# Optimization experiments

Hardware: AMD Instinct MI355X
Metric: run time of the kernel (lower is better)

Reference implementation:

```python
import jax, jax.numpy as jnp
import numpy as np

WAY, SHOT, P, FDIM, HDIM, NHEADS = 5, 5, 10, 640, 512, 8
H = W = 14
NUM_SPT = WAY * SHOT
EPS_BN = 1e-5
EPS_LN = 1e-5


def _l2norm(x, axis=-1):
    n = jnp.linalg.norm(x, axis=axis, keepdims=True)
    return x / jnp.maximum(n, 1e-12)


def _cbr(x, Wc, bc, g, beta):
    # 1x1 conv + BatchNorm(train stats) + ReLU. x: [N,C,H,W], Wc: [O,C]
    y = jnp.einsum('nchw,oc->nohw', x, Wc) + bc[None, :, None, None]
    mu = y.mean((0, 2, 3))
    var = y.var((0, 2, 3))
    y = (y - mu[None, :, None, None]) / jnp.sqrt(var[None, :, None, None] + EPS_BN)
    y = y * g[None, :, None, None] + beta[None, :, None, None]
    return jax.nn.relu(y)


def _mha(x, Wq, bq, Wk, bk, Wv, bv, Wa, ba, ln_g, ln_b):
    B, S, D = x.shape
    dk = D // NHEADS
    def proj(Wt, bt):
        return (x @ Wt.T + bt).reshape(B, S, NHEADS, dk).transpose(0, 2, 1, 3)
    q, k, v = proj(Wq, bq), proj(Wk, bk), proj(Wv, bv)
    scores = jnp.einsum('bhqd,bhkd->bhqk', q, k) / jnp.sqrt(jnp.asarray(dk, x.dtype))
    att = jax.nn.softmax(scores, axis=-1)
    ctx = jnp.einsum('bhqk,bhkd->bhqd', att, v).transpose(0, 2, 1, 3).reshape(B, S, D)
    out = ctx @ Wa.T + ba + x  # residual
    mu = out.mean(-1, keepdims=True)
    var = out.var(-1, keepdims=True)
    return ((out - mu) / jnp.sqrt(var + EPS_LN)) * ln_g + ln_b


def setup_inputs() -> dict:
    k = jax.random.key(0)
    ks = jax.random.split(k, 16)
    s = 0.02
    return {
        'key':   jax.random.normal(ks[0], (NUM_SPT + 75, FDIM, H, W), jnp.float32),
        'query': jax.random.normal(ks[1], (75, FDIM, H, W), jnp.float32),
        'Wc':  jax.random.normal(ks[2], (HDIM, FDIM), jnp.float32) * s,
        'bc':  jnp.zeros((HDIM,), jnp.float32),
        'g1':  jnp.ones((HDIM,), jnp.float32),
        'b1':  jnp.zeros((HDIM,), jnp.float32),
        'Wq':  jax.random.normal(ks[3], (HDIM, HDIM), jnp.float32) * s,
        'bq':  jnp.zeros((HDIM,), jnp.float32),
        'Wk':  jax.random.normal(ks[4], (HDIM, HDIM), jnp.float32) * s,
        'bk':  jnp.zeros((HDIM,), jnp.float32),
        'Wv':  jax.random.normal(ks[5], (HDIM, HDIM), jnp.float32) * s,
        'bv':  jnp.zeros((HDIM,), jnp.float32),
        'Wa':  jax.random.normal(ks[6], (HDIM, HDIM), jnp.float32) * s,
        'ba':  jnp.zeros((HDIM,), jnp.float32),
        'ln_g': jnp.ones((HDIM,), jnp.float32),
        'ln_b': jnp.zeros((HDIM,), jnp.float32),
        'Wm':  jax.random.normal(ks[7], (P, HDIM), jnp.float32) * s,
        'Wo':  jax.random.normal(ks[8], (FDIM, HDIM), jnp.float32) * s,
        'bo':  jnp.zeros((FDIM,), jnp.float32),
        'g2':  jnp.ones((FDIM,), jnp.float32),
        'b2':  jnp.zeros((FDIM,), jnp.float32),
    }


def reference(key, query, Wc, bc, g1, b1, Wq, bq, Wk, bk, Wv, bv, Wa, ba, ln_g, ln_b, Wm, Wo, bo, g2, b2):
    # proto_concept: conv1x1 + BN + ReLU
    key_ = _cbr(key, Wc, bc, g1, b1)                 # [B, HDIM, H, W]
    B, D, h, w = key_.shape
    feats = key_.transpose(0, 2, 3, 1).reshape(B, h * w, D)
    support = feats[:NUM_SPT].reshape(SHOT, WAY, h * w, D).mean(0)   # [WAY, hw, D]
    qf = feats[NUM_SPT:]                                             # [NQ, hw, D]
    nq = B - NUM_SPT

    support = _mha(support, Wq, bq, Wk, bk, Wv, bv, Wa, ba, ln_g, ln_b)
    qf = _mha(qf, Wq, bq, Wk, bk, Wv, bv, Wa, ba, ln_g, ln_b)

    # prototype formation: softmax over all support positions (dim 0)
    mw = (support @ Wm.T).reshape(-1, P, 1)          # [WAY*hw, P, 1]
    mw = jax.nn.softmax(mw, axis=0)
    sflat = support.reshape(-1, D)                   # [WAY*hw, D]
    protos = (mw * sflat[:, None, :]).sum(0)         # [P, D]

    # ---- query_loss (training branch) ----
    protos_n = _l2norm(protos)                       # [P, D]

    # diversity loss (faithful to original incl. triu over (P, D) dims)
    diff2 = (protos_n[None, :, :] - protos_n[:, None, :]) ** 2   # [P, P, D]
    dis = 1.0 - diff2[None]                                      # [1, P, P, D]
    dis = dis * (dis > 0).astype(dis.dtype)
    tri = jnp.triu(jnp.ones((P, D), dis.dtype), k=1)
    dis = dis * tri
    dis_loss = (dis.sum(1).sum(1) * 2.0 / (P * (P - 1))).mean()

    cst_loss = ((protos_n[1:] - protos_n[:-1]) ** 2).sum(-1).mean()

    # dual-softmax scoring (protos shared across batch)
    score = jnp.einsum('bnd,md->bnm', qf, protos_n)  # [NQ, hw, P]
    sp = jax.nn.softmax(score, axis=-1)
    new_q = _l2norm(jnp.einsum('bnm,md->bnd', sp, protos_n))

    idx = jnp.argmax(score, axis=-1)                 # top-1 proto per position
    pos = protos_n[idx]                              # [NQ, hw, D]
    fea_loss = jnp.mean((qf - pos) ** 2)

    uq = new_q.transpose(0, 2, 1).reshape(nq, D, h, w)
    updated = _cbr(uq, Wo, bo, g2, b2) + query       # [NQ, FDIM, H, W]
    return (updated, fea_loss, cst_loss, dis_loss)
```

## Files before the change

kernel.cpp:

```cpp
#include <hip/hip_runtime.h>
#include <math.h>

#define WAYS 5
#define SHOTS 5
#define PP 10
#define FDIMC 640
#define HD 512
#define SEQ 196
#define NB 100
#define NQB 75
#define NMHA 80
#define M1 (NB*SEQ)
#define MMHA (NMHA*SEQ)
#define MQ (NQB*SEQ)
#define NBLK_ROWK (MQ/4)
#define OUT_UPD (NQB*FDIMC*SEQ)

#define OFF_CS1S 0
#define OFF_CS1Q 512
#define OFF_CS2S 1024
#define OFF_CS2Q 1664
#define ZERO_FLOATS 2306
#define OFF_ST1SC 2308
#define OFF_ST1SH 2820
#define OFF_ST2SC 3332
#define OFF_ST2SH 3972
#define OFF_M    4612
#define OFF_PN   14412

#define RB 20480
#define RC (RB + 15439360)
#define RD (RC + 8028160)
#define RE (RD + 8028160)
#define RF (RE + 8028160)
#define RG (RF + 4014080)
#define RH (RG + 4014080)
#define OFF_XOUT (RB + 10000000)
#define OFF_FEAP (RF + 3763200)
#define OFF_WSM  RG
#define OFF_PPART (RG + 16384)

typedef __bf16 bf16x8 __attribute__((ext_vector_type(8)));
typedef float f32x4 __attribute__((ext_vector_type(4)));

__device__ __forceinline__ ushort f2bf(float f) {
  unsigned u = __float_as_uint(f);
  return (ushort)((u + 0x7fffu + ((u >> 16) & 1u)) >> 16);
}
__device__ __forceinline__ float bf2f(ushort u) {
  return __uint_as_float(((unsigned)u) << 16);
}

__device__ __forceinline__ f32x4 mfma16(bf16x8 a, bf16x8 b, f32x4 c) {
  return __builtin_amdgcn_mfma_f32_16x16x32_bf16(a, b, c, 0, 0, 0);
}

__device__ __forceinline__ float waveSum(float v) {
#pragma unroll
  for (int o = 32; o; o >>= 1) v += __shfl_xor(v, o, 64);
  return v;
}


__global__ __launch_bounds__(256) void key_transpose(const float* __restrict__ key,
                                                     ushort* __restrict__ keyT) {
  __shared__ float T[32][33];
  const int n = blockIdx.z, c0 = blockIdx.y*32, s0 = blockIdx.x*32;
  const int tj = threadIdx.x & 31, ti = threadIdx.x >> 5;
#pragma unroll
  for (int it = 0; it < 4; ++it) {
    const int cl = it*8 + ti;
    const int s = s0 + tj;
    T[cl][tj] = (s < SEQ) ? key[((size_t)n*FDIMC + c0 + cl)*SEQ + s] : 0.f;
  }
  __syncthreads();
#pragma unroll
  for (int it = 0; it < 4; ++it) {
    const int sl = it*8 + ti;
    const int s = s0 + sl;
    if (s < SEQ) keyT[((size_t)(n*SEQ + s))*FDIMC + c0 + tj] = f2bf(T[tj][sl]);
  }
}

__global__ void wconvert(const float* __restrict__ Wc, const float* __restrict__ Wq,
                         const float* __restrict__ Wk, const float* __restrict__ Wv,
                         const float* __restrict__ Wa, const float* __restrict__ Wo,
                         ushort* __restrict__ wh) {
  const int i = blockIdx.x*256 + threadIdx.x;
  float v;
  if (i < 327680) v = Wc[i];
  else if (i < 589824) v = Wq[i - 327680];
  else if (i < 851968) v = Wk[i - 589824];
  else if (i < 1114112) v = Wv[i - 851968];
  else if (i < 1376256) v = Wa[i - 1114112];
  else v = Wo[i - 1376256];
  wh[i] = f2bf(v);
}

template<int OM, int CS>
__global__ __launch_bounds__(256) void gemm_bf(const ushort* __restrict__ A,
    const ushort* __restrict__ W, const float* __restrict__ bias,
    float* __restrict__ Cf, ushort* __restrict__ Ch, int M, int N, int K,
    float* __restrict__ gsum, float* __restrict__ gsq) {
  __shared__ ushort As[128*32];
  __shared__ ushort Bs[128*32];
  __shared__ float csum[128], csq[128];
  const int tid = threadIdx.x;
  const int m0 = blockIdx.y*128, n0 = blockIdx.x*128;
  const int w = tid >> 6, lane = tid & 63;
  const int wr = w >> 1, wc = w & 1;
  const int g = lane >> 4, c = lane & 15;

  const int ch0 = tid, ch1 = 256 + tid;
  const int ar0 = ch0 >> 2, ar1 = ch1 >> 2;
  const int ak0 = (ch0 & 3) * 8, ak1 = (ch1 & 3) * 8;
  int gr0 = m0 + ar0; if (gr0 > M-1) gr0 = M-1;
  int gr1 = m0 + ar1; if (gr1 > M-1) gr1 = M-1;
  const ushort* Ap0 = A + (size_t)gr0*K + ak0;
  const ushort* Ap1 = A + (size_t)gr1*K + ak1;
  const ushort* Wp0 = W + (size_t)(n0 + ar0)*K + ak0;
  const ushort* Wp1 = W + (size_t)(n0 + ar1)*K + ak1;

  f32x4 acc[4][4];
#pragma unroll
  for (int i = 0; i < 4; ++i)
#pragma unroll
    for (int j = 0; j < 4; ++j) acc[i][j] = (f32x4)(0.0f);

  for (int k0 = 0; k0 < K; k0 += 32) {
    const uint4 a0 = *(const uint4*)(Ap0 + k0);
    const uint4 a1 = *(const uint4*)(Ap1 + k0);
    const uint4 b0 = *(const uint4*)(Wp0 + k0);
    const uint4 b1 = *(const uint4*)(Wp1 + k0);
    __syncthreads();
    *(uint4*)(&As[ch0*8]) = a0;
    *(uint4*)(&As[ch1*8]) = a1;
    *(uint4*)(&Bs[ch0*8]) = b0;
    *(uint4*)(&Bs[ch1*8]) = b1;
    __syncthreads();
    bf16x8 af[4], bfr[4];
#pragma unroll
    for (int mi = 0; mi < 4; ++mi)
      af[mi] = *(const bf16x8*)(&As[(wr*64 + mi*16 + c)*32 + g*8]);
#pragma unroll
    for (int ni = 0; ni < 4; ++ni)
      bfr[ni] = *(const bf16x8*)(&Bs[(wc*64 + ni*16 + c)*32 + g*8]);
#pragma unroll
    for (int mi = 0; mi < 4; ++mi)
#pragma unroll
      for (int ni = 0; ni < 4; ++ni)
        acc[mi][ni] = mfma16(af[mi], bfr[ni], acc[mi][ni]);
  }

  if (CS) {
    __syncthreads();
    if (tid < 128) { csum[tid] = 0.f; csq[tid] = 0.f; }
    __syncthreads();
  }

#pragma unroll
  for (int ni = 0; ni < 4; ++ni) {
    const int col = n0 + wc*64 + ni*16 + c;
    const float bb = bias[col];
    float ls = 0.f, lq = 0.f;
#pragma unroll
    for (int mi = 0; mi < 4; ++mi) {
#pragma unroll
      for (int q = 0; q < 4; ++q) {
        const int row = m0 + wr*64 + mi*16 + g*4 + q;
        if (row < M) {
          const float v = acc[mi][ni][q] + bb;
          if (OM == 0) Cf[(size_t)row*N + col] = v;
          else if (OM == 1) Ch[(size_t)row*N + col] = f2bf(v);
          else Ch[(size_t)row*N + col] = f2bf(v*0.125f);
          if (CS) { ls += v; lq += v*v; }
        }
      }
    }
    if (CS) {
      const int lcol = wc*64 + ni*16 + c;
      atomicAdd(&csum[lcol], ls);
      atomicAdd(&csq[lcol], lq);
    }
  }
  if (CS) {
    __syncthreads();
    if (tid < 128) {
      atomicAdd(&gsum[n0 + tid], csum[tid]);
      atomicAdd(&gsq[n0 + tid], csq[tid]);
    }
  }
}


__global__ void bn_finalize(const float* __restrict__ sums, const float* __restrict__ sumsq,
    const float* __restrict__ g, const float* __restrict__ b, int C, float invM,
    float* __restrict__ scale, float* __restrict__ shift) {
  const int c = blockIdx.x*256 + threadIdx.x;
  if (c >= C) return;
  const float mu = sums[c]*invM;
  const float var = sumsq[c]*invM - mu*mu;
  const float sc = rsqrtf(var + 1e-5f) * g[c];
  scale[c] = sc;
  shift[c] = b[c] - mu*sc;
}

__global__ __launch_bounds__(256) void bn1_apply(const ushort* __restrict__ y1,
    const float* __restrict__ scale, const float* __restrict__ shift,
    ushort* __restrict__ srawh, ushort* __restrict__ xbufh) {
  const int i8 = blockIdx.x*256 + threadIdx.x;
  if (i8 >= M1*HD/8) return;
  const int e = i8 << 3;
  const int col = e & (HD - 1);
  const uint4 raw = ((const uint4*)y1)[i8];
  unsigned rw[4] = {raw.x, raw.y, raw.z, raw.w};
  unsigned res[4];
#pragma unroll
  for (int j = 0; j < 4; ++j) {
    float v0 = bf2f((ushort)(rw[j] & 0xffffu));
    float v1 = bf2f((ushort)(rw[j] >> 16));
    v0 = fmaxf(fmaf(v0, scale[col + 2*j],     shift[col + 2*j]),     0.f);
    v1 = fmaxf(fmaf(v1, scale[col + 2*j + 1], shift[col + 2*j + 1]), 0.f);
    res[j] = (unsigned)f2bf(v0) | ((unsigned)f2bf(v1) << 16);
  }
  const uint4 o = make_uint4(res[0], res[1], res[2], res[3]);
  if (e < 25*SEQ*HD) ((uint4*)srawh)[i8] = o;
  else ((uint4*)xbufh)[i8 - (20*SEQ*HD/8)] = o;
}

__global__ void support_mean(const ushort* __restrict__ srawh, ushort* __restrict__ xbufh) {
  const int i8 = blockIdx.x*256 + threadIdx.x;
  if (i8 >= WAYS*SEQ*HD/8) return;
  const int e = i8 << 3;
  const int w = e / (SEQ*HD);
  const int rem = e - w*(SEQ*HD);
  float acc[8] = {};
#pragma unroll
  for (int s = 0; s < SHOTS; ++s) {
    const uint4 v = *(const uint4*)(srawh + (size_t)(s*WAYS + w)*(SEQ*HD) + rem);
    const unsigned rw[4] = {v.x, v.y, v.z, v.w};
#pragma unroll
    for (int j = 0; j < 4; ++j) {
      acc[2*j]   += bf2f((ushort)(rw[j] & 0xffffu));
      acc[2*j+1] += bf2f((ushort)(rw[j] >> 16));
    }
  }
  unsigned res[4];
#pragma unroll
  for (int j = 0; j < 4; ++j)
    res[j] = (unsigned)f2bf(acc[2*j]*0.2f) | ((unsigned)f2bf(acc[2*j+1]*0.2f) << 16);
  ((uint4*)xbufh)[i8] = make_uint4(res[0], res[1], res[2], res[3]);
}


__global__ __launch_bounds__(256) void attn_qk(const ushort* __restrict__ qb,
    const ushort* __restrict__ kb, ushort* __restrict__ P) {
  __shared__ ushort Ks[208*72];
  const int bh = blockIdx.x, b = bh >> 3, h = bh & 7;
  const int tid = threadIdx.x;
  for (int idx = tid; idx < 208*8; idx += 256) {
    const int row = idx >> 3, part = idx & 7;
    uint4 v = make_uint4(0u,0u,0u,0u);
    if (row < SEQ) v = *(const uint4*)(kb + ((size_t)(b*SEQ + row))*HD + h*64 + part*8);
    *(uint4*)(&Ks[row*72 + part*8]) = v;
  }
  __syncthreads();
  const int w = tid >> 6, lane = tid & 63, g = lane >> 4, c = lane & 15;
  for (int rt = w; rt < 13; rt += 4) {
    int qrow = b*SEQ + rt*16 + c; if (qrow > MMHA-1) qrow = MMHA-1;
    const bf16x8 aq0 = *(const bf16x8*)(qb + (size_t)qrow*HD + h*64 + g*8);
    const bf16x8 aq1 = *(const bf16x8*)(qb + (size_t)qrow*HD + h*64 + 32 + g*8);
    f32x4 acc[13];
#pragma unroll
    for (int ct = 0; ct < 13; ++ct) acc[ct] = (f32x4)(0.0f);
#pragma unroll
    for (int ct = 0; ct < 13; ++ct) {
      const bf16x8 b0 = *(const bf16x8*)(&Ks[(ct*16 + c)*72 + g*8]);
      const bf16x8 b1 = *(const bf16x8*)(&Ks[(ct*16 + c)*72 + 32 + g*8]);
      acc[ct] = mfma16(aq0, b0, acc[ct]);
      acc[ct] = mfma16(aq1, b1, acc[ct]);
    }
    if (c >= 4) acc[12] = (f32x4)(-1e30f);
    float mrow[4], Z[4];
#pragma unroll
    for (int q = 0; q < 4; ++q) {
      float mx = acc[0][q];
#pragma unroll
      for (int ct = 1; ct < 13; ++ct) mx = fmaxf(mx, acc[ct][q]);
      mrow[q] = mx;
    }
#pragma unroll
    for (int q = 0; q < 4; ++q) {
#pragma unroll
      for (int msk = 1; msk < 16; msk <<= 1)
        mrow[q] = fmaxf(mrow[q], __shfl_xor(mrow[q], msk, 64));
    }
#pragma unroll
    for (int q = 0; q < 4; ++q) Z[q] = 0.f;
#pragma unroll
    for (int ct = 0; ct < 13; ++ct)
#pragma unroll
      for (int q = 0; q < 4; ++q) {
        const float e = __expf(acc[ct][q] - mrow[q]);
        acc[ct][q] = e; Z[q] += e;
      }
#pragma unroll
    for (int q = 0; q < 4; ++q) {
#pragma unroll
      for (int msk = 1; msk < 16; msk <<= 1) Z[q] += __shfl_xor(Z[q], msk, 64);
      Z[q] = 1.f / Z[q];
    }
    const size_t pb = (size_t)bh*(208*232);
#pragma unroll
    for (int q = 0; q < 4; ++q) {
      ushort* pr = P + pb + (size_t)(rt*16 + g*4 + q)*232;
#pragma unroll
      for (int ct = 0; ct < 13; ++ct) pr[ct*16 + c] = f2bf(acc[ct][q]*Z[q]);
      pr[208 + c] = 0;
      if (c < 8) pr[224 + c] = 0;
    }
  }
}


__global__ __launch_bounds__(256) void v_transpose(const ushort* __restrict__ vb,
                                                   ushort* __restrict__ VT) {
  __shared__ ushort Vs[196*72];
  const int bh = blockIdx.x, b = bh >> 3, h = bh & 7;
  const int tid = threadIdx.x;
  for (int idx = tid; idx < 196*8; idx += 256) {
    const int row = idx >> 3, part = idx & 7;
    *(uint4*)(&Vs[row*72 + part*8]) =
        *(const uint4*)(vb + ((size_t)(b*SEQ + row))*HD + h*64 + part*8);
  }
  __syncthreads();
  ushort* o = VT + (size_t)bh*64*224;
  for (int idx = tid; idx < 64*224; idx += 256) {
    const int d = idx/224, s = idx - d*224;
    o[idx] = (s < SEQ) ? Vs[s*72 + d] : (ushort)0;
  }
}


__global__ __launch_bounds__(256) void attn_pv(const ushort* __restrict__ P,
    const ushort* __restrict__ VT, ushort* __restrict__ ctx) {
  __shared__ ushort Ps[112*232];
  const int bh = blockIdx.x, b = bh >> 3, h = bh & 7;
  const int tid = threadIdx.x, w = tid >> 6, lane = tid & 63, g = lane >> 4, c = lane & 15;
  bf16x8 bv[7];
  const ushort* vt = VT + (size_t)bh*64*224 + (size_t)(w*16 + c)*224;
#pragma unroll
  for (int ks = 0; ks < 7; ++ks) bv[ks] = *(const bf16x8*)(vt + ks*32 + g*8);
  const char* pg = (const char*)(P + (size_t)bh*(208*232));
#pragma unroll
  for (int half = 0; half < 2; ++half) {
    const int r0 = half ? 112 : 0;
    const int nbytes = half ? 96*464 : 112*464;
    __syncthreads();
    for (int byte = tid*16; byte < nbytes; byte += 4096)
      *(uint4*)((char*)Ps + byte) = *(const uint4*)(pg + r0*464 + byte);
    __syncthreads();
    const int rtlo = half ? 7 : 0, rthi = half ? 13 : 7;
    for (int rt = rtlo; rt < rthi; ++rt) {
      const int lrow = rt*16 - r0 + c;
      f32x4 acc = (f32x4)(0.0f);
#pragma unroll
      for (int ks = 0; ks < 7; ++ks) {
        const bf16x8 a = *(const bf16x8*)(&Ps[lrow*232 + ks*32 + g*8]);
        acc = mfma16(a, bv[ks], acc);
      }
#pragma unroll
      for (int q = 0; q < 4; ++q) {
        const int srow = rt*16 + g*4 + q;
        if (srow < SEQ)
          ctx[((size_t)(b*SEQ + srow))*HD + h*64 + w*16 + c] = f2bf(acc[q]);
      }
    }
  }
}


__global__ __launch_bounds__(256) void ln_kernel(const float* __restrict__ tmp,
    const ushort* __restrict__ xin, const float* __restrict__ g,
    const float* __restrict__ bta, ushort* __restrict__ outh) {
  const int row = blockIdx.x*4 + (threadIdx.x >> 6);
  const int lane = threadIdx.x & 63;
  const float* t = tmp + (size_t)row*HD;
  const ushort* x = xin + (size_t)row*HD;
  float v[8]; float s = 0.f;
#pragma unroll
  for (int i = 0; i < 8; ++i) {
    const float val = t[i*64 + lane] + bf2f(x[i*64 + lane]);
    v[i] = val; s += val;
  }
  s = waveSum(s);
  const float mu = s * (1.f/HD);
  float sq = 0.f;
#pragma unroll
  for (int i = 0; i < 8; ++i) { const float d = v[i] - mu; sq += d*d; }
  sq = waveSum(sq);
  const float istd = rsqrtf(sq*(1.f/HD) + 1e-5f);
#pragma unroll
  for (int i = 0; i < 8; ++i) {
    const int d = i*64 + lane;
    outh[(size_t)row*HD + d] = f2bf((v[i] - mu)*istd*g[d] + bta[d]);
  }
}


__global__ __launch_bounds__(256) void mw_kernel(const ushort* __restrict__ xout,
    const float* __restrict__ Wm, float* __restrict__ m) {
  const int row = blockIdx.x*4 + (threadIdx.x >> 6);
  const int lane = threadIdx.x & 63;
  const ushort* x = xout + (size_t)row*HD;
  float xv[8];
#pragma unroll
  for (int i = 0; i < 8; ++i) xv[i] = bf2f(x[i*64 + lane]);
#pragma unroll
  for (int p = 0; p < PP; ++p) {
    const float* wp = Wm + p*HD;
    float s = 0.f;
#pragma unroll
    for (int i = 0; i < 8; ++i) s = fmaf(xv[i], wp[i*64 + lane], s);
    s = waveSum(s);
    if (lane == 0) m[row*PP + p] = s;
  }
}

__global__ __launch_bounds__(256) void wsm_kernel(const float* __restrict__ m,
                                                  float* __restrict__ wsm) {
  __shared__ float red[256];
  const int p = blockIdx.x, tid = threadIdx.x;
  float lmax = -1e30f;
  for (int r = tid; r < 980; r += 256) lmax = fmaxf(lmax, m[r*PP + p]);
  red[tid] = lmax; __syncthreads();
  for (int s = 128; s; s >>= 1) { if (tid < s) red[tid] = fmaxf(red[tid], red[tid+s]); __syncthreads(); }
  const float bmax = red[0]; __syncthreads();
  float lsum = 0.f;
  for (int r = tid; r < 980; r += 256) {
    const float e = __expf(m[r*PP + p] - bmax);
    wsm[p*980 + r] = e; lsum += e;
  }
  red[tid] = lsum; __syncthreads();
  for (int s = 128; s; s >>= 1) { if (tid < s) red[tid] += red[tid+s]; __syncthreads(); }
  const float invZ = 1.f / red[0];
  for (int r = tid; r < 980; r += 256) wsm[p*980 + r] *= invZ;
}

__global__ __launch_bounds__(256) void protos_part(const float* __restrict__ wsm,
    const ushort* __restrict__ xout, float* __restrict__ part) {
  const int p = blockIdx.y, chunk = blockIdx.x, tid = threadIdx.x;
  const int r0 = chunk*49;
  float a0 = 0.f, a1 = 0.f;
  for (int r = r0; r < r0 + 49; ++r) {
    const float w = wsm[p*980 + r];
    a0 = fmaf(w, bf2f(xout[(size_t)r*HD + tid]), a0);
    a1 = fmaf(w, bf2f(xout[(size_t)r*HD + tid + 256]), a1);
  }
  float* o = part + (((size_t)p*20 + chunk) << 9);
  o[tid] = a0;
  o[tid + 256] = a1;
}

__global__ __launch_bounds__(256) void protos_fin(const float* __restrict__ part,
                                                  float* __restrict__ pn) {
  __shared__ float red[256];
  const int p = blockIdx.x, tid = threadIdx.x;
  float a0 = 0.f, a1 = 0.f;
  for (int cch = 0; cch < 20; ++cch) {
    const float* o = part + (((size_t)p*20 + cch) << 9);
    a0 += o[tid];
    a1 += o[tid + 256];
  }
  red[tid] = a0*a0 + a1*a1; __syncthreads();
  for (int s = 128; s; s >>= 1) { if (tid < s) red[tid] += red[tid+s]; __syncthreads(); }
  const float rn = 1.f / fmaxf(sqrtf(red[0]), 1e-12f);
  pn[p*HD + tid] = a0*rn;
  pn[p*HD + tid + 256] = a1*rn;
}

__global__ __launch_bounds__(256) void losses_kernel(const float* __restrict__ pn, float* __restrict__ out) {
  __shared__ float redc[256], redd[256];
  const int tid = threadIdx.x;
  float cpart = 0.f, dpart = 0.f;
  for (int d = tid; d < HD; d += 256) {
    float a[PP];
#pragma unroll
    for (int j = 0; j < PP; ++j) a[j] = pn[j*HD + d];
#pragma unroll
    for (int j = 0; j < PP; ++j) {
      if (d > j) {
#pragma unroll
        for (int i = 0; i < PP; ++i) {
          const float df = a[j] - a[i];
          const float t = 1.f - df*df;
          if (t > 0.f) dpart += t;
        }
      }
    }
#pragma unroll
    for (int j = 0; j < PP - 1; ++j) { const float df = a[j+1] - a[j]; cpart += df*df; }
  }
  redc[tid] = cpart; redd[tid] = dpart; __syncthreads();
  for (int s = 128; s; s >>= 1) {
    if (tid < s) { redc[tid] += redc[tid+s]; redd[tid] += redd[tid+s]; }
    __syncthreads();
  }
  if (tid == 0) {
    out[OUT_UPD + 1] = redc[0] / 9.f;
    out[OUT_UPD + 2] = redd[0] * (2.f / (90.f * 512.f));
  }
}

__global__ __launch_bounds__(256) void rowk(const ushort* __restrict__ xout, const float* __restrict__ pn,
    ushort* __restrict__ newq, float* __restrict__ feapart) {
  __shared__ float Ps[PP*HD];
  __shared__ float fred[4];
  const int tid = threadIdx.x;
  for (int idx = tid; idx < PP*HD; idx += 256) Ps[idx] = pn[idx];
  __syncthreads();
  const int row = blockIdx.x*4 + (tid >> 6);
  const int lane = tid & 63;
  const ushort* x = xout + (size_t)(WAYS*SEQ + row)*HD;
  float xv[8];
#pragma unroll
  for (int i = 0; i < 8; ++i) xv[i] = bf2f(x[i*64 + lane]);
  float sc[PP];
#pragma unroll
  for (int p = 0; p < PP; ++p) {
    float s = 0.f;
#pragma unroll
    for (int i = 0; i < 8; ++i) s = fmaf(xv[i], Ps[p*HD + i*64 + lane], s);
    sc[p] = waveSum(s);
  }
  float mx = sc[0]; int am = 0;
#pragma unroll
  for (int p = 1; p < PP; ++p) if (sc[p] > mx) { mx = sc[p]; am = p; }
  float Z = 0.f; float sp[PP];
#pragma unroll
  for (int p = 0; p < PP; ++p) { const float e = expf(sc[p] - mx); sp[p] = e; Z += e; }
  const float rz = 1.f / Z;
  float nv[8]; float ss = 0.f;
#pragma unroll
  for (int i = 0; i < 8; ++i) {
    float a = 0.f;
#pragma unroll
    for (int p = 0; p < PP; ++p) a = fmaf(sp[p], Ps[p*HD + i*64 + lane], a);
    a *= rz; nv[i] = a; ss += a*a;
  }
  ss = waveSum(ss);
  const float rn = 1.f / fmaxf(sqrtf(ss), 1e-12f);
#pragma unroll
  for (int i = 0; i < 8; ++i) newq[(size_t)row*HD + i*64 + lane] = f2bf(nv[i]*rn);
  float fp = 0.f;
#pragma unroll
  for (int i = 0; i < 8; ++i) { const float d = xv[i] - Ps[am*HD + i*64 + lane]; fp += d*d; }
  fp = waveSum(fp);
  if (lane == 0) fred[tid >> 6] = fp;
  __syncthreads();
  if (tid == 0) feapart[blockIdx.x] = fred[0] + fred[1] + fred[2] + fred[3];
}

__global__ __launch_bounds__(256) void fea_finalize(const float* __restrict__ feapart,
                                                    float* __restrict__ out) {
  __shared__ float red[256];
  float s = 0.f;
  for (int i = threadIdx.x; i < NBLK_ROWK; i += 256) s += feapart[i];
  red[threadIdx.x] = s; __syncthreads();
  for (int st = 128; st; st >>= 1) {
    if (threadIdx.x < st) red[threadIdx.x] += red[threadIdx.x + st];
    __syncthreads();
  }
  if (threadIdx.x == 0) out[OUT_UPD] = red[0] / (float)((size_t)NQB*SEQ*HD);
}

__global__ __launch_bounds__(256) void bn2_apply(const float* __restrict__ y2, const float* __restrict__ scale,
    const float* __restrict__ shift, const float* __restrict__ query, float* __restrict__ out) {
  __shared__ float tile[32][33];
  const int n = blockIdx.z, o0 = blockIdx.y*32, hw0 = blockIdx.x*32;
  const int tj = threadIdx.x & 31, ti = threadIdx.x >> 5;
#pragma unroll
  for (int it = 0; it < 4; ++it) {
    const int hw = hw0 + it*8 + ti;
    const int o = o0 + tj;
    float v = 0.f;
    if (hw < SEQ) v = fmaxf(fmaf(y2[((size_t)n*SEQ + hw)*FDIMC + o], scale[o], shift[o]), 0.f);
    tile[it*8 + ti][tj] = v;
  }
  __syncthreads();
#pragma unroll
  for (int it = 0; it < 4; ++it) {
    const int o = o0 + it*8 + ti;
    const int hw = hw0 + tj;
    if (hw < SEQ) {
      const size_t oi = ((size_t)n*FDIMC + o)*SEQ + hw;
      out[oi] = tile[tj][it*8 + ti] + query[oi];
    }
  }
}

extern "C" void kernel_launch(void* const* d_in, const int* in_sizes, int n_in,
                              void* d_out, int out_size, void* d_ws, size_t ws_size,
                              hipStream_t stream) {
  const float* key   = (const float*)d_in[0];
  const float* query = (const float*)d_in[1];
  const float* Wc    = (const float*)d_in[2];
  const float* bc    = (const float*)d_in[3];
  const float* g1    = (const float*)d_in[4];
  const float* b1    = (const float*)d_in[5];
  const float* Wq    = (const float*)d_in[6];
  const float* bq    = (const float*)d_in[7];
  const float* Wk    = (const float*)d_in[8];
  const float* bk    = (const float*)d_in[9];
  const float* Wv    = (const float*)d_in[10];
  const float* bv    = (const float*)d_in[11];
  const float* Wa    = (const float*)d_in[12];
  const float* ba    = (const float*)d_in[13];
  const float* ln_g  = (const float*)d_in[14];
  const float* ln_b  = (const float*)d_in[15];
  const float* Wm    = (const float*)d_in[16];
  const float* Wo    = (const float*)d_in[17];
  const float* bo    = (const float*)d_in[18];
  const float* g2    = (const float*)d_in[19];
  const float* b2    = (const float*)d_in[20];
  float* out = (float*)d_out;
  float* w = (float*)d_ws;

  ushort* y1h   = (ushort*)(w + RB);
  ushort* P     = (ushort*)(w + RB);
  float*  y2f   = w + RB;
  ushort* xouth = (ushort*)(w + OFF_XOUT);
  ushort* VT    = (ushort*)(w + RC);
  ushort* keyT  = (ushort*)(w + RD);
  ushort* qb    = (ushort*)(w + RD);
  float*  tmpf  = w + RD;
  ushort* xbufh = (ushort*)(w + RE);
  ushort* srawh = (ushort*)(w + RF);
  ushort* kb    = (ushort*)(w + RF);
  ushort* newq  = (ushort*)(w + RF);
  ushort* vb    = (ushort*)(w + RG);
  ushort* ctx   = (ushort*)(w + RG);
  ushort* wh    = (ushort*)(w + RH);
  float*  feapart = w + OFF_FEAP;
  float*  wsm   = w + OFF_WSM;
  float*  ppart = w + OFF_PPART;
  ushort* Wcb = wh;
  ushort* Wqb = wh + 327680;
  ushort* Wkb = wh + 589824;
  ushort* Wvb = wh + 851968;
  ushort* Wab = wh + 1114112;
  ushort* Wob = wh + 1376256;

  hipMemsetAsync(w, 0, ZERO_FLOATS*sizeof(float), stream);

  key_transpose<<<dim3(7, 20, NB), 256, 0, stream>>>(key, keyT);
  wconvert<<<6656, 256, 0, stream>>>(Wc, Wq, Wk, Wv, Wa, Wo, wh);

  gemm_bf<1,1><<<dim3(4, 154), 256, 0, stream>>>(keyT, Wcb, bc, nullptr, y1h, M1, HD, FDIMC,
                                                 w + OFF_CS1S, w + OFF_CS1Q);
  bn_finalize<<<2, 256, 0, stream>>>(w + OFF_CS1S, w + OFF_CS1Q, g1, b1, HD, 1.f/M1,
                                     w + OFF_ST1SC, w + OFF_ST1SH);
  bn1_apply<<<M1*HD/8/256, 256, 0, stream>>>(y1h, w + OFF_ST1SC, w + OFF_ST1SH, srawh, xbufh);
  support_mean<<<WAYS*SEQ*HD/8/256, 256, 0, stream>>>(srawh, xbufh);

  gemm_bf<2,0><<<dim3(4, 123), 256, 0, stream>>>(xbufh, Wqb, bq, nullptr, qb, MMHA, HD, HD, nullptr, nullptr);
  gemm_bf<1,0><<<dim3(4, 123), 256, 0, stream>>>(xbufh, Wkb, bk, nullptr, kb, MMHA, HD, HD, nullptr, nullptr);
  gemm_bf<1,0><<<dim3(4, 123), 256, 0, stream>>>(xbufh, Wvb, bv, nullptr, vb, MMHA, HD, HD, nullptr, nullptr);

  v_transpose<<<NMHA*8, 256, 0, stream>>>(vb, VT);
  attn_qk<<<NMHA*8, 256, 0, stream>>>(qb, kb, P);
  attn_pv<<<NMHA*8, 256, 0, stream>>>(P, VT, ctx);

  gemm_bf<0,0><<<dim3(4, 123), 256, 0, stream>>>(ctx, Wab, ba, tmpf, nullptr, MMHA, HD, HD, nullptr, nullptr);
  ln_kernel<<<MMHA/4, 256, 0, stream>>>(tmpf, xbufh, ln_g, ln_b, xouth);

  mw_kernel<<<245, 256, 0, stream>>>(xouth, Wm, w + OFF_M);
  wsm_kernel<<<PP, 256, 0, stream>>>(w + OFF_M, wsm);
  protos_part<<<dim3(20, PP), 256, 0, stream>>>(wsm, xouth, ppart);
  protos_fin<<<PP, 256, 0, stream>>>(ppart, w + OFF_PN);
  losses_kernel<<<1, 256, 0, stream>>>(w + OFF_PN, out);
  rowk<<<NBLK_ROWK, 256, 0, stream>>>(xouth, w + OFF_PN, newq, feapart);

  gemm_bf<0,1><<<dim3(5, 115), 256, 0, stream>>>(newq, Wob, bo, y2f, nullptr, MQ, FDIMC, HD,
                                                 w + OFF_CS2S, w + OFF_CS2Q);
  bn_finalize<<<3, 256, 0, stream>>>(w + OFF_CS2S, w + OFF_CS2Q, g2, b2, FDIMC, 1.f/MQ,
                                     w + OFF_ST2SC, w + OFF_ST2SH);
  fea_finalize<<<1, 256, 0, stream>>>(feapart, out);
  bn2_apply<<<dim3(7, 20, NQB), 256, 0, stream>>>(y2f, w + OFF_ST2SC, w + OFF_ST2SH, query, out);
}
```

Measured before the change: 381.0 us.

## Use direct global-to-LDS loads and XCD-aware block remapping in GEMM

Replaces register-staged global loads plus LDS stores in the bf16 GEMM with global_load_lds instructions that write straight into shared memory. It also remaps workgroup IDs so consecutive tiles land on the same XCD chunk, improving L2 reuse. This removes VGPR staging and ds_write instructions. However, loads are now issued after the barrier, so prefetch overlap with the previous iteration's compute is lost.

Measured after the change: 370.4 us. -2.8%, faster.

```diff
diff --git a/kernel.cpp b/kernel.cpp
--- a/kernel.cpp
+++ b/kernel.cpp
@@ -61,6 +61,13 @@
   return v;
 }
 
+__device__ __forceinline__ void gld16(const void* g, void* l) {
+  __builtin_amdgcn_global_load_lds(
+      (const __attribute__((address_space(1))) void*)g,
+      (__attribute__((address_space(3))) void*)l,
+      16, 0, 0);
+}
+
 
 __global__ __launch_bounds__(256) void key_transpose(const float* __restrict__ key,
                                                      ushort* __restrict__ keyT) {
@@ -106,20 +113,33 @@
   __shared__ ushort Bs[128*32];
   __shared__ float csum[128], csq[128];
   const int tid = threadIdx.x;
-  const int m0 = blockIdx.y*128, n0 = blockIdx.x*128;
+
+  const int nwg = gridDim.x * gridDim.y;
+  int flat = blockIdx.y * gridDim.x + blockIdx.x;
+  {
+    const int q = nwg >> 3, r = nwg & 7;
+    const int j = flat & 7, t = flat >> 3;
+    flat = (j < r ? j*(q+1) : r*(q+1) + (j-r)*q) + t;
+  }
+  const int m0 = (flat / gridDim.x) * 128;
+  const int n0 = (flat % gridDim.x) * 128;
+
   const int w = tid >> 6, lane = tid & 63;
   const int wr = w >> 1, wc = w & 1;
   const int g = lane >> 4, c = lane & 15;
 
-  const int ch0 = tid, ch1 = 256 + tid;
-  const int ar0 = ch0 >> 2, ar1 = ch1 >> 2;
-  const int ak0 = (ch0 & 3) * 8, ak1 = (ch1 & 3) * 8;
-  int gr0 = m0 + ar0; if (gr0 > M-1) gr0 = M-1;
-  int gr1 = m0 + ar1; if (gr1 > M-1) gr1 = M-1;
-  const ushort* Ap0 = A + (size_t)gr0*K + ak0;
-  const ushort* Ap1 = A + (size_t)gr1*K + ak1;
-  const ushort* Wp0 = W + (size_t)(n0 + ar0)*K + ak0;
-  const ushort* Wp1 = W + (size_t)(n0 + ar1)*K + ak1;
+  const int srow = w*16 + (lane >> 2);
+  const int sk   = (lane & 3) * 8;
+  int ar0 = m0 + srow;       if (ar0 > M-1) ar0 = M-1;
+  int ar1 = m0 + 64 + srow;  if (ar1 > M-1) ar1 = M-1;
+  const ushort* Ap0 = A + (size_t)ar0*K + sk;
+  const ushort* Ap1 = A + (size_t)ar1*K + sk;
+  const ushort* Bp0 = W + (size_t)(n0 + srow)*K + sk;
+  const ushort* Bp1 = W + (size_t)(n0 + 64 + srow)*K + sk;
+  ushort* lA0 = &As[w*512];
+  ushort* lA1 = &As[(4+w)*512];
+  ushort* lB0 = &Bs[w*512];
+  ushort* lB1 = &Bs[(4+w)*512];
 
   f32x4 acc[4][4];
 #pragma unroll
@@ -128,15 +148,11 @@
     for (int j = 0; j < 4; ++j) acc[i][j] = (f32x4)(0.0f);
 
   for (int k0 = 0; k0 < K; k0 += 32) {
-    const uint4 a0 = *(const uint4*)(Ap0 + k0);
-    const uint4 a1 = *(const uint4*)(Ap1 + k0);
-    const uint4 b0 = *(const uint4*)(Wp0 + k0);
-    const uint4 b1 = *(const uint4*)(Wp1 + k0);
-    __syncthreads();
-    *(uint4*)(&As[ch0*8]) = a0;
-    *(uint4*)(&As[ch1*8]) = a1;
-    *(uint4*)(&Bs[ch0*8]) = b0;
-    *(uint4*)(&Bs[ch1*8]) = b1;
+    __syncthreads();
+    gld16(Ap0 + k0, lA0);
+    gld16(Ap1 + k0, lA1);
+    gld16(Bp0 + k0, lB0);
+    gld16(Bp1 + k0, lB1);
     __syncthreads();
     bf16x8 af[4], bfr[4];
 #pragma unroll
```
